# Kernel optimization log

Hardware: AMD Instinct MI355X
Metric: run time of the kernel (lower is better)

Reference implementation:

```python
import jax, jax.numpy as jnp
import numpy as np


def setup_inputs() -> dict:
    key = jax.random.key(0)
    ks = jax.random.split(key, 16)
    B, T, H = 64, 512, 256
    s = lambda n: 1.0 / np.sqrt(n)
    return {
        "q_vec": jax.random.normal(ks[0], (B, H), jnp.float32),
        "fact_vecs": jax.random.normal(ks[1], (B, T, H), jnp.float32),
        "input_len": jax.random.randint(ks[2], (B,), 1, T + 1, jnp.int32),
        "W1": jax.random.normal(ks[3], (7 * H, H), jnp.float32) * s(7 * H),
        "b1": jnp.zeros((H,), jnp.float32),
        "W2": jax.random.normal(ks[4], (H, 1), jnp.float32) * s(H),
        "b2": jnp.zeros((1,), jnp.float32),
        "Wr": jax.random.normal(ks[5], (H, H), jnp.float32) * s(H),
        "Ur": jax.random.normal(ks[6], (H, H), jnp.float32) * s(H),
        "br": jnp.zeros((H,), jnp.float32),
        "Wh": jax.random.normal(ks[7], (H, H), jnp.float32) * s(H),
        "Uh": jax.random.normal(ks[8], (H, H), jnp.float32) * s(H),
        "bh": jnp.zeros((H,), jnp.float32),
        "Ws": jax.random.normal(ks[9], (2 * H, 1), jnp.float32) * s(2 * H),
        "bs": jnp.zeros((1,), jnp.float32),
        "We": jax.random.normal(ks[10], (2 * H, 1), jnp.float32) * s(2 * H),
        "be": jnp.zeros((1,), jnp.float32),
    }


def reference(q_vec, fact_vecs, input_len, W1, b1, W2, b2,
              Wr, Ur, br, Wh, Uh, bh, Ws, bs, We, be):
    B, T, H = fact_vecs.shape
    m = q_vec  # prev_memory = q_vec (never actually updated in the original inference loop)
    qb = jnp.broadcast_to(q_vec[:, None, :], (B, T, H))
    mb = qb  # m == q_vec
    f = fact_vecs
    # episodic attention features: [f, m, q, f*q, f*m, |f-q|, |f-m|] -> [B,T,7H]
    feats = jnp.concatenate(
        [f, mb, qb, f * qb, f * mb, jnp.abs(f - qb), jnp.abs(f - mb)], axis=-1)
    att = jnp.tanh(feats @ W1 + b1) @ W2 + b2          # [B,T,1]
    g = jax.nn.softmax(att[..., 0], axis=1)            # [B,T]

    # AttentionGRU scan over time with sequence-length masking (dynamic_rnn semantics)
    valid = (jnp.arange(T)[:, None] < input_len[None, :])  # [T,B]

    def step(h, inp):
        x_t, g_t, v_t = inp  # [B,H], [B], [B]
        r = jax.nn.sigmoid(x_t @ Wr + h @ Ur + br)
        hc = jnp.tanh(x_t @ Wh + (r * h) @ Uh + bh)
        hn = g_t[:, None] * hc + (1.0 - g_t[:, None]) * h
        hn = jnp.where(v_t[:, None], hn, h)
        out = jnp.where(v_t[:, None], hn, jnp.zeros_like(hn))
        return hn, out

    xs = (jnp.swapaxes(fact_vecs, 0, 1), g.T, valid)
    _, outs = jax.lax.scan(step, jnp.zeros((B, H), fact_vecs.dtype), xs)
    e_outputs = jnp.swapaxes(outs, 0, 1)               # [B,T,H]

    # predict_position (final hop, is_iteration=False): tanh dense over [prev_memory, e_t]
    cat = jnp.concatenate([jnp.broadcast_to(m[:, None, :], (B, T, H)), e_outputs], axis=-1)
    out_s = jnp.tanh(cat @ Ws + bs)[..., 0]            # [B,T]
    out_e = jnp.tanh(cat @ We + be)[..., 0]            # [B,T]
    return out_s, out_e
```

## Files before the change

### kernel.cpp

```cpp
#include <hip/hip_runtime.h>
#include <cstddef>


static __device__ __forceinline__ float b2f(unsigned short u) {
  return __uint_as_float(((unsigned)u) << 16);
}
static __device__ __forceinline__ float blo(unsigned w) { return __uint_as_float(w << 16); }
static __device__ __forceinline__ float bhi(unsigned w) { return __uint_as_float(w & 0xffff0000u); }
static __device__ __forceinline__ unsigned short f2b(float f) {
  unsigned u = __float_as_uint(f);
  u += 0x7fffu + ((u >> 16) & 1u);
  return (unsigned short)(u >> 16);
}
static __device__ __forceinline__ float ldf(const void* b, size_t i, int md) {
  return md ? ((const float*)b)[i] : b2f(((const unsigned short*)b)[i]);
}
static __device__ __forceinline__ unsigned short ldb(const void* b, size_t i, int md) {
  return md ? f2b(((const float*)b)[i]) : ((const unsigned short*)b)[i];
}

typedef short bfrag __attribute__((ext_vector_type(8)));
typedef float f32x4 __attribute__((ext_vector_type(4)));

template <int CTRL>
static __device__ __forceinline__ float dpp_add(float x) {
  int v = __builtin_amdgcn_update_dpp(0, __float_as_int(x), CTRL, 0xF, 0xF, true);
  return x + __int_as_float(v);
}
static __device__ __forceinline__ float red16(float x) {
  x = dpp_add<0xB1>(x);
  x = dpp_add<0x4E>(x);
  x = dpp_add<0x141>(x);
  x = dpp_add<0x140>(x);
  return x;
}
static __device__ __forceinline__ void sync_lds() {
  __builtin_amdgcn_fence(__ATOMIC_RELEASE, "workgroup", "local");
  __builtin_amdgcn_s_barrier();
  __builtin_amdgcn_fence(__ATOMIC_ACQUIRE, "workgroup", "local");
}
static __device__ __forceinline__ float fast_tanh(float x) {
  float xc = fminf(fmaxf(x, -15.f), 15.f);
  return 1.f - 2.f * __builtin_amdgcn_rcpf(__expf(2.f * xc) + 1.f);
}

__global__ void k_detect(const void* __restrict__ fact, int* __restrict__ mode) {
  int tid = threadIdx.x;
  const unsigned short* u = (const unsigned short*)fact;
  float v = fabsf(b2f(u[2 * tid]));
  if (!(v == v)) v = 1e30f;
  for (int o = 32; o > 0; o >>= 1) v = fmaxf(v, __shfl_xor(v, o));
  __shared__ float red[4];
  int wave = tid >> 6, lane = tid & 63;
  if (lane == 0) red[wave] = v;
  __syncthreads();
  if (tid == 0) {
    float m = fmaxf(fmaxf(red[0], red[1]), fmaxf(red[2], red[3]));
    mode[0] = (m > 1e4f) ? 1 : 0;
  }
}

__global__ void k_prep_w(const void* __restrict__ W1,
                         const void* __restrict__ Wr,
                         const void* __restrict__ Wh,
                         const void* __restrict__ Ur,
                         const void* __restrict__ Uh,
                         const int* __restrict__ mode,
                         unsigned* __restrict__ W5q,
                         unsigned* __restrict__ Urp,
                         unsigned* __restrict__ Uhp) {
  int md = *mode;
  int idx = blockIdx.x * 256 + threadIdx.x;
  int i = idx >> 8, j = idx & 255;
  Urp[idx] = (unsigned)ldb(Ur, (size_t)(2 * i) * 256 + j, md) |
             ((unsigned)ldb(Ur, (size_t)(2 * i + 1) * 256 + j, md) << 16);
  Uhp[idx] = (unsigned)ldb(Uh, (size_t)(2 * i) * 256 + j, md) |
             ((unsigned)ldb(Uh, (size_t)(2 * i + 1) * 256 + j, md) << 16);
  float v0, v1;
  int p;
  p = i;
  v0 = ldf(W1, (size_t)(2 * i) * 256 + j, md);
  v1 = ldf(W1, (size_t)(2 * i + 1) * 256 + j, md);
  W5q[(((p >> 2) * 256 + j) << 2) + (p & 3)] = (unsigned)f2b(v0) | ((unsigned)f2b(v1) << 16);
  p = 128 + i;
  v0 = ldf(W1, (size_t)(768 + 2 * i) * 256 + j, md) + ldf(W1, (size_t)(1024 + 2 * i) * 256 + j, md);
  v1 = ldf(W1, (size_t)(769 + 2 * i) * 256 + j, md) + ldf(W1, (size_t)(1025 + 2 * i) * 256 + j, md);
  W5q[(((p >> 2) * 256 + j) << 2) + (p & 3)] = (unsigned)f2b(v0) | ((unsigned)f2b(v1) << 16);
  p = 256 + i;
  v0 = ldf(W1, (size_t)(1280 + 2 * i) * 256 + j, md) + ldf(W1, (size_t)(1536 + 2 * i) * 256 + j, md);
  v1 = ldf(W1, (size_t)(1281 + 2 * i) * 256 + j, md) + ldf(W1, (size_t)(1537 + 2 * i) * 256 + j, md);
  W5q[(((p >> 2) * 256 + j) << 2) + (p & 3)] = (unsigned)f2b(v0) | ((unsigned)f2b(v1) << 16);
  p = 384 + i;
  v0 = ldf(Wr, (size_t)(2 * i) * 256 + j, md);
  v1 = ldf(Wr, (size_t)(2 * i + 1) * 256 + j, md);
  W5q[(((p >> 2) * 256 + j) << 2) + (p & 3)] = (unsigned)f2b(v0) | ((unsigned)f2b(v1) << 16);
  p = 512 + i;
  v0 = ldf(Wh, (size_t)(2 * i) * 256 + j, md);
  v1 = ldf(Wh, (size_t)(2 * i + 1) * 256 + j, md);
  W5q[(((p >> 2) * 256 + j) << 2) + (p & 3)] = (unsigned)f2b(v0) | ((unsigned)f2b(v1) << 16);
}

__global__ void k_prep_q(const void* __restrict__ q,
                         const void* __restrict__ W1,
                         const void* __restrict__ b1,
                         const void* __restrict__ Ws,
                         const void* __restrict__ bs,
                         const void* __restrict__ We,
                         const void* __restrict__ be,
                         const int* __restrict__ mode,
                         float* __restrict__ qw1,
                         float* __restrict__ qs,
                         float* __restrict__ qe) {
  __shared__ float qsh[256];
  __shared__ float reds[4], rede[4];
  int md = *mode;
  int b = blockIdx.x, tid = threadIdx.x;
  float qv = ldf(q, (size_t)b * 256 + tid, md);
  qsh[tid] = qv;
  __syncthreads();
  float acc = ldf(b1, tid, md);
  for (int i = 0; i < 256; ++i) {
    float w = ldf(W1, (size_t)(256 + i) * 256 + tid, md) + ldf(W1, (size_t)(512 + i) * 256 + tid, md);
    acc = fmaf(qsh[i], w, acc);
  }
  qw1[b * 256 + tid] = acc;
  float ps = qv * ldf(Ws, tid, md);
  float pe = qv * ldf(We, tid, md);
  for (int o = 32; o > 0; o >>= 1) { ps += __shfl_down(ps, o); pe += __shfl_down(pe, o); }
  int wave = tid >> 6, lane = tid & 63;
  if (lane == 0) { reds[wave] = ps; rede[wave] = pe; }
  __syncthreads();
  if (tid == 0) {
    qs[b] = ldf(bs, 0, md) + reds[0] + reds[1] + reds[2] + reds[3];
    qe[b] = ldf(be, 0, md) + rede[0] + rede[1] + rede[2] + rede[3];
  }
}

__launch_bounds__(256, 2)
__global__ void k_main(const void* __restrict__ fact,
                       const void* __restrict__ q,
                       const unsigned* __restrict__ W5q,
                       const float* __restrict__ qw1,
                       const void* __restrict__ W2,
                       const void* __restrict__ b2v,
                       const void* __restrict__ br,
                       const void* __restrict__ bh,
                       const int* __restrict__ mode,
                       float* __restrict__ att,
                       unsigned* __restrict__ xrh) {
  __shared__ __align__(16) unsigned short A[16 * 776];
  __shared__ float wsc[64];
  int md = *mode;
  int blk = blockIdx.x;
  int b = blk >> 5, t0 = (blk & 31) * 16;
  int tid = threadIdx.x;
  {
    float qv = ldf(q, (size_t)b * 256 + tid, md);
    for (int r = 0; r < 16; ++r) {
      float f = ldf(fact, ((size_t)(b * 512 + t0 + r)) * 256 + tid, md);
      A[r * 776 + tid] = f2b(f);
      A[r * 776 + 256 + tid] = f2b(f * qv);
      A[r * 776 + 512 + tid] = f2b(fabsf(f - qv));
    }
  }
  __syncthreads();
  int wv = tid >> 6, lane = tid & 63;
  int n16 = lane & 15, quad = lane >> 4;
  int colb = wv * 64 + n16;
  const uint4* W4 = (const uint4*)W5q;
  f32x4 z = {0.f, 0.f, 0.f, 0.f};
  f32x4 u[4] = {z, z, z, z}, ar[4] = {z, z, z, z}, ah[4] = {z, z, z, z};
#pragma unroll
  for (int kc = 0; kc < 8; ++kc) {
    uint4 av = *(const uint4*)((const char*)A + n16 * 1552 + kc * 64 + quad * 16);
    bfrag af = __builtin_bit_cast(bfrag, av);
    int pg = kc * 4 + quad;
#pragma unroll
    for (int tile = 0; tile < 4; ++tile) {
      int col = colb + tile * 16;
      uint4 bu = W4[(size_t)pg * 256 + col];
      uint4 bw = W4[(size_t)(96 + pg) * 256 + col];
      uint4 bv = W4[(size_t)(128 + pg) * 256 + col];
      u[tile] = __builtin_amdgcn_mfma_f32_16x16x32_bf16(af, __builtin_bit_cast(bfrag, bu), u[tile], 0, 0, 0);
      ar[tile] = __builtin_amdgcn_mfma_f32_16x16x32_bf16(af, __builtin_bit_cast(bfrag, bw), ar[tile], 0, 0, 0);
      ah[tile] = __builtin_amdgcn_mfma_f32_16x16x32_bf16(af, __builtin_bit_cast(bfrag, bv), ah[tile], 0, 0, 0);
    }
  }
#pragma unroll
  for (int kc = 8; kc < 24; ++kc) {
    uint4 av = *(const uint4*)((const char*)A + n16 * 1552 + kc * 64 + quad * 16);
    bfrag af = __builtin_bit_cast(bfrag, av);
    int pg = kc * 4 + quad;
#pragma unroll
    for (int tile = 0; tile < 4; ++tile) {
      int col = colb + tile * 16;
      uint4 bu = W4[(size_t)pg * 256 + col];
      u[tile] = __builtin_amdgcn_mfma_f32_16x16x32_bf16(af, __builtin_bit_cast(bfrag, bu), u[tile], 0, 0, 0);
    }
  }
  float qwv[4], w2v[4], brv[4], bhv[4];
#pragma unroll
  for (int tile = 0; tile < 4; ++tile) {
    int col = colb + tile * 16;
    qwv[tile] = qw1[b * 256 + col];
    w2v[tile] = ldf(W2, col, md);
    brv[tile] = ldf(br, col, md);
    bhv[tile] = ldf(bh, col, md);
  }
  float ps[4];
#pragma unroll
  for (int reg = 0; reg < 4; ++reg) {
    float p = 0.f;
#pragma unroll
    for (int tile = 0; tile < 4; ++tile) {
      float hid = fast_tanh(u[tile][reg] + qwv[tile]);
      p = fmaf(hid, w2v[tile], p);
    }
    ps[reg] = red16(p);
  }
  if (n16 == 0) {
#pragma unroll
    for (int reg = 0; reg < 4; ++reg) wsc[wv * 16 + quad * 4 + reg] = ps[reg];
  }
  __syncthreads();
  if (tid < 16) {
    att[b * 512 + t0 + tid] =
        wsc[tid] + wsc[16 + tid] + wsc[32 + tid] + wsc[48 + tid] + ldf(b2v, 0, md);
  }
#pragma unroll
  for (int tile = 0; tile < 4; ++tile) {
    int col = colb + tile * 16;
#pragma unroll
    for (int reg = 0; reg < 4; ++reg) {
      int t = t0 + quad * 4 + reg;
      unsigned v = (unsigned)f2b(ar[tile][reg] + brv[tile]) |
                   ((unsigned)f2b(ah[tile][reg] + bhv[tile]) << 16);
      xrh[((size_t)(b * 512 + t)) * 256 + col] = v;
    }
  }
}

__global__ void k_softmax(const float* __restrict__ att, float* __restrict__ g) {
  __shared__ float red[8];
  int b = blockIdx.x, tid = threadIdx.x;
  float v = att[b * 512 + tid];
  float m = v;
  for (int o = 32; o > 0; o >>= 1) m = fmaxf(m, __shfl_xor(m, o));
  int wave = tid >> 6, lane = tid & 63;
  if (lane == 0) red[wave] = m;
  __syncthreads();
  m = red[0];
#pragma unroll
  for (int w = 1; w < 8; ++w) m = fmaxf(m, red[w]);
  float e = __expf(v - m);
  float s = e;
  for (int o = 32; o > 0; o >>= 1) s += __shfl_xor(s, o);
  __syncthreads();
  if (lane == 0) red[wave] = s;
  __syncthreads();
  s = red[0] + red[1] + red[2] + red[3] + red[4] + red[5] + red[6] + red[7];
  g[b * 512 + tid] = e / s;
}

__launch_bounds__(512, 2)
__global__ void k_scan(const unsigned* __restrict__ Urp,
                       const unsigned* __restrict__ Uhp,
                       const unsigned* __restrict__ xrh,
                       const float* __restrict__ g,
                       const int* __restrict__ input_len,
                       unsigned short* __restrict__ ep) {
  __shared__ __align__(16) unsigned short hB[4 * 272];
  __shared__ __align__(16) unsigned short rhB[4 * 272];
  int b0 = blockIdx.x * 4;
  int tid = threadIdx.x;
  int wv = tid >> 6, lane = tid & 63;
  int n16 = lane & 15, quad = lane >> 4;
  int col0 = wv * 32 + n16;
  int col1 = col0 + 16;
  uint4 br4[2][8], bh4[2][8];
#pragma unroll
  for (int tile = 0; tile < 2; ++tile) {
    int col = wv * 32 + tile * 16 + n16;
#pragma unroll
    for (int kc = 0; kc < 8; ++kc) {
      int p = kc * 16 + quad * 4;
      uint4 rv = {Urp[(size_t)p * 256 + col], Urp[(size_t)(p + 1) * 256 + col],
                  Urp[(size_t)(p + 2) * 256 + col], Urp[(size_t)(p + 3) * 256 + col]};
      uint4 hv = {Uhp[(size_t)p * 256 + col], Uhp[(size_t)(p + 1) * 256 + col],
                  Uhp[(size_t)(p + 2) * 256 + col], Uhp[(size_t)(p + 3) * 256 + col]};
      br4[tile][kc] = rv;
      bh4[tile][kc] = hv;
    }
  }
  for (int i = tid; i < 4 * 272; i += 512) { hB[i] = 0; rhB[i] = 0; }
  int mylen = input_len[b0 + quad];
  float hm0 = 0.f, hm1 = 0.f;
  const char* hbase = (const char*)hB + (n16 >> 2) * 544 + quad * 16;
  const char* rhbase = (const char*)rhB + (n16 >> 2) * 544 + quad * 16;
  const unsigned* xrow = xrh + (size_t)(b0 + quad) * 512 * 256;
  const float* grow = g + (size_t)(b0 + quad) * 512;
  unsigned short* eprow = ep + (size_t)(b0 + quad) * 512 * 256;

  unsigned xa[16], xbb[16];
  float4 ga0, ga1, gb0, gb1;
  auto prefetch = [&](int tb, unsigned (&xr)[16], float4& g0, float4& g1) {
    const unsigned* xp = xrow + (size_t)tb * 8 * 256;
#pragma unroll
    for (int s = 0; s < 8; ++s) {
      xr[2 * s] = xp[s * 256 + col0];
      xr[2 * s + 1] = xp[s * 256 + col1];
    }
    const float* gp = grow + tb * 8;
    g0 = *(const float4*)gp;
    g1 = *(const float4*)(gp + 4);
  };
  prefetch(0, xa, ga0, ga1);
  __syncthreads();
  const f32x4 z4 = {0.f, 0.f, 0.f, 0.f};

  auto step = [&](int T, unsigned XC0, unsigned XC1, float GT) {
    f32x4 accA[2][4];
#pragma unroll
    for (int tl = 0; tl < 2; ++tl)
#pragma unroll
      for (int j = 0; j < 4; ++j) accA[tl][j] = z4;
#pragma unroll
    for (int kc = 0; kc < 8; ++kc) {
      uint4 av = *(const uint4*)(hbase + kc * 64);
      bfrag af = __builtin_bit_cast(bfrag, av);
      int j = kc & 3;
      accA[0][j] = __builtin_amdgcn_mfma_f32_16x16x32_bf16(af, __builtin_bit_cast(bfrag, br4[0][kc]), accA[0][j], 0, 0, 0);
      accA[1][j] = __builtin_amdgcn_mfma_f32_16x16x32_bf16(af, __builtin_bit_cast(bfrag, br4[1][kc]), accA[1][j], 0, 0, 0);
    }
    {
      float v0 = (accA[0][0][0] + accA[0][1][0]) + (accA[0][2][0] + accA[0][3][0]);
      float v1 = (accA[1][0][0] + accA[1][1][0]) + (accA[1][2][0] + accA[1][3][0]);
      float e0 = __expf(-(v0 + blo(XC0)));
      float e1 = __expf(-(v1 + blo(XC1)));
      float r0 = __builtin_amdgcn_rcpf(1.f + e0);
      float r1 = __builtin_amdgcn_rcpf(1.f + e1);
      rhB[quad * 272 + col0] = f2b(r0 * hm0);
      rhB[quad * 272 + col1] = f2b(r1 * hm1);
    }
    sync_lds();
    f32x4 accB[2][4];
#pragma unroll
    for (int tl = 0; tl < 2; ++tl)
#pragma unroll
      for (int j = 0; j < 4; ++j) accB[tl][j] = z4;
#pragma unroll
    for (int kc = 0; kc < 8; ++kc) {
      uint4 av = *(const uint4*)(rhbase + kc * 64);
      bfrag af = __builtin_bit_cast(bfrag, av);
      int j = kc & 3;
      accB[0][j] = __builtin_amdgcn_mfma_f32_16x16x32_bf16(af, __builtin_bit_cast(bfrag, bh4[0][kc]), accB[0][j], 0, 0, 0);
      accB[1][j] = __builtin_amdgcn_mfma_f32_16x16x32_bf16(af, __builtin_bit_cast(bfrag, bh4[1][kc]), accB[1][j], 0, 0, 0);
    }
    {
      float w0 = (accB[0][0][0] + accB[0][1][0]) + (accB[0][2][0] + accB[0][3][0]);
      float w1 = (accB[1][0][0] + accB[1][1][0]) + (accB[1][2][0] + accB[1][3][0]);
      float c0 = fminf(fmaxf(w0 + bhi(XC0), -15.f), 15.f);
      float c1 = fminf(fmaxf(w1 + bhi(XC1), -15.f), 15.f);
      float hc0 = 1.f - 2.f * __builtin_amdgcn_rcpf(__expf(2.f * c0) + 1.f);
      float hc1 = 1.f - 2.f * __builtin_amdgcn_rcpf(__expf(2.f * c1) + 1.f);
      bool valid = T < mylen;
      float hn0 = hm0 + GT * (hc0 - hm0);
      float hn1 = hm1 + GT * (hc1 - hm1);
      hm0 = valid ? hn0 : hm0;
      hm1 = valid ? hn1 : hm1;
      unsigned short hb0 = f2b(hm0), hb1 = f2b(hm1);
      hB[quad * 272 + col0] = hb0;
      hB[quad * 272 + col1] = hb1;
      eprow[(size_t)T * 256 + col0] = valid ? hb0 : (unsigned short)0;
      eprow[(size_t)T * 256 + col1] = valid ? hb1 : (unsigned short)0;
    }
    sync_lds();
  };

  for (int tb2 = 0; tb2 < 32; ++tb2) {
    prefetch(2 * tb2 + 1, xbb, gb0, gb1);
#pragma unroll
    for (int tt = 0; tt < 8; ++tt)
      step(tb2 * 16 + tt, xa[2 * tt], xa[2 * tt + 1], tt < 4 ? ga0[tt] : ga1[tt - 4]);
    prefetch(tb2 < 31 ? 2 * tb2 + 2 : 63, xa, ga0, ga1);
#pragma unroll
    for (int tt = 0; tt < 8; ++tt)
      step(tb2 * 16 + 8 + tt, xbb[2 * tt], xbb[2 * tt + 1], tt < 4 ? gb0[tt] : gb1[tt - 4]);
  }
}

__global__ void k_out(const unsigned short* __restrict__ ep,
                      const void* __restrict__ Ws,
                      const void* __restrict__ We,
                      const float* __restrict__ qs,
                      const float* __restrict__ qe,
                      const int* __restrict__ mode,
                      float* __restrict__ out) {
  int md = *mode;
  int tid = threadIdx.x;
  int wave = tid >> 6, lane = tid & 63;
  int row = blockIdx.x * 4 + wave;
  const unsigned short* er = ep + (size_t)row * 256 + lane * 4;
  float f0 = b2f(er[0]), f1 = b2f(er[1]), f2 = b2f(er[2]), f3 = b2f(er[3]);
  int n = 256 + lane * 4;
  float s = f0 * ldf(Ws, n, md) + f1 * ldf(Ws, n + 1, md) + f2 * ldf(Ws, n + 2, md) + f3 * ldf(Ws, n + 3, md);
  float e = f0 * ldf(We, n, md) + f1 * ldf(We, n + 1, md) + f2 * ldf(We, n + 2, md) + f3 * ldf(We, n + 3, md);
  for (int o = 32; o > 0; o >>= 1) { s += __shfl_down(s, o); e += __shfl_down(e, o); }
  if (lane == 0) {
    int b = row >> 9;
    out[row] = tanhf(qs[b] + s);
    out[32768 + row] = tanhf(qe[b] + e);
  }
}

extern "C" void kernel_launch(void* const* d_in, const int* in_sizes, int n_in,
                              void* d_out, int out_size, void* d_ws, size_t ws_size,
                              hipStream_t stream) {
  const void* q    = d_in[0];
  const void* fact = d_in[1];
  const int* ilen  = (const int*)d_in[2];
  const void* W1   = d_in[3];
  const void* b1   = d_in[4];
  const void* W2   = d_in[5];
  const void* b2v  = d_in[6];
  const void* Wr   = d_in[7];
  const void* Ur   = d_in[8];
  const void* br   = d_in[9];
  const void* Wh   = d_in[10];
  const void* Uh   = d_in[11];
  const void* bh   = d_in[12];
  const void* Ws   = d_in[13];
  const void* bs   = d_in[14];
  const void* We   = d_in[15];
  const void* be   = d_in[16];

  char* w = (char*)d_ws;
  unsigned* W5q = (unsigned*)(w);
  unsigned* Urp = (unsigned*)(w + 1310720);
  unsigned* Uhp = (unsigned*)(w + 1441792);
  float*    qw1 = (float*)(w + 1572864);
  float*    qs  = (float*)(w + 1638400);
  float*    qe  = (float*)(w + 1638656);
  float*    att = (float*)(w + 1638912);
  float*    g   = (float*)(w + 1769984);
  unsigned* xrh = (unsigned*)(w + 1901056);
  unsigned short* ep = (unsigned short*)(w + 35455488);
  int*      mode = (int*)(w + 52232704);
  float* out = (float*)d_out;

  k_detect<<<dim3(1), dim3(256), 0, stream>>>(fact, mode);
  k_prep_w<<<dim3(128), dim3(256), 0, stream>>>(W1, Wr, Wh, Ur, Uh, mode, W5q, Urp, Uhp);
  k_prep_q<<<dim3(64), dim3(256), 0, stream>>>(q, W1, b1, Ws, bs, We, be, mode, qw1, qs, qe);
  k_main<<<dim3(2048), dim3(256), 0, stream>>>(fact, q, W5q, qw1, W2, b2v, br, bh, mode, att, xrh);
  k_softmax<<<dim3(64), dim3(512), 0, stream>>>(att, g);
  k_scan<<<dim3(16), dim3(512), 0, stream>>>(Urp, Uhp, xrh, g, ilen, ep);
  k_out<<<dim3(8192), dim3(256), 0, stream>>>(ep, Ws, We, qs, qe, mode, out);
}
```

Before: 678.0 us.

## Halve scan block to 4 waves, each covering 64 hidden columns

The recurrent scan kernel now runs 256 threads per block, so each wave handles four 16-column tiles instead of two. The Ur/Uh weight fragments held in registers double, and the accumulation uses two partial accumulators per tile instead of four. Fewer waves should make the two per-step LDS barriers cheaper and reuse each loaded h fragment across more MFMAs. The cost is more serial MFMA work per wave on the critical path and higher register pressure, which could cause spills.

```diff
diff --git a/kernel.cpp b/kernel.cpp
--- a/kernel.cpp
+++ b/kernel.cpp
@@ -262,7 +262,7 @@
   g[b * 512 + tid] = e / s;
 }
 
-__launch_bounds__(512, 2)
+__launch_bounds__(256, 1)
 __global__ void k_scan(const unsigned* __restrict__ Urp,
                        const unsigned* __restrict__ Uhp,
                        const unsigned* __restrict__ xrh,
@@ -275,12 +275,11 @@
   int tid = threadIdx.x;
   int wv = tid >> 6, lane = tid & 63;
   int n16 = lane & 15, quad = lane >> 4;
-  int col0 = wv * 32 + n16;
-  int col1 = col0 + 16;
-  uint4 br4[2][8], bh4[2][8];
-#pragma unroll
-  for (int tile = 0; tile < 2; ++tile) {
-    int col = wv * 32 + tile * 16 + n16;
+  int colb = wv * 64 + n16;
+  uint4 br4[4][8], bh4[4][8];
+#pragma unroll
+  for (int tile = 0; tile < 4; ++tile) {
+    int col = colb + tile * 16;
 #pragma unroll
     for (int kc = 0; kc < 8; ++kc) {
       int p = kc * 16 + quad * 4;
@@ -292,9 +291,9 @@
       bh4[tile][kc] = hv;
     }
   }
-  for (int i = tid; i < 4 * 272; i += 512) { hB[i] = 0; rhB[i] = 0; }
+  for (int i = tid; i < 4 * 272; i += 256) { hB[i] = 0; rhB[i] = 0; }
   int mylen = input_len[b0 + quad];
-  float hm0 = 0.f, hm1 = 0.f;
+  float hm[4] = {0.f, 0.f, 0.f, 0.f};
   const char* hbase = (const char*)hB + (n16 >> 2) * 544 + quad * 16;
   const char* rhbase = (const char*)rhB + (n16 >> 2) * 544 + quad * 16;
   const unsigned* xrow = xrh + (size_t)(b0 + quad) * 512 * 256;
@@ -302,90 +301,78 @@
   unsigned short* eprow = ep + (size_t)(b0 + quad) * 512 * 256;
 
   unsigned xa[16], xbb[16];
-  float4 ga0, ga1, gb0, gb1;
-  auto prefetch = [&](int tb, unsigned (&xr)[16], float4& g0, float4& g1) {
-    const unsigned* xp = xrow + (size_t)tb * 8 * 256;
-#pragma unroll
-    for (int s = 0; s < 8; ++s) {
-      xr[2 * s] = xp[s * 256 + col0];
-      xr[2 * s + 1] = xp[s * 256 + col1];
-    }
-    const float* gp = grow + tb * 8;
-    g0 = *(const float4*)gp;
-    g1 = *(const float4*)(gp + 4);
+  float4 ga, gb;
+  auto prefetch = [&](int tb, unsigned (&xr)[16], float4& gq) {
+    const unsigned* xp = xrow + (size_t)tb * 4 * 256;
+#pragma unroll
+    for (int s = 0; s < 4; ++s)
+#pragma unroll
+      for (int tl = 0; tl < 4; ++tl)
+        xr[s * 4 + tl] = xp[s * 256 + colb + tl * 16];
+    gq = *(const float4*)(grow + tb * 4);
   };
-  prefetch(0, xa, ga0, ga1);
+  prefetch(0, xa, ga);
   __syncthreads();
   const f32x4 z4 = {0.f, 0.f, 0.f, 0.f};
 
-  auto step = [&](int T, unsigned XC0, unsigned XC1, float GT) {
-    f32x4 accA[2][4];
-#pragma unroll
-    for (int tl = 0; tl < 2; ++tl)
-#pragma unroll
-      for (int j = 0; j < 4; ++j) accA[tl][j] = z4;
+  auto step = [&](int T, unsigned X0, unsigned X1, unsigned X2, unsigned X3, float GT) {
+    unsigned XC[4] = {X0, X1, X2, X3};
+    f32x4 accA[4][2];
+#pragma unroll
+    for (int tl = 0; tl < 4; ++tl) { accA[tl][0] = z4; accA[tl][1] = z4; }
 #pragma unroll
     for (int kc = 0; kc < 8; ++kc) {
       uint4 av = *(const uint4*)(hbase + kc * 64);
       bfrag af = __builtin_bit_cast(bfrag, av);
-      int j = kc & 3;
-      accA[0][j] = __builtin_amdgcn_mfma_f32_16x16x32_bf16(af, __builtin_bit_cast(bfrag, br4[0][kc]), accA[0][j], 0, 0, 0);
-      accA[1][j] = __builtin_amdgcn_mfma_f32_16x16x32_bf16(af, __builtin_bit_cast(bfrag, br4[1][kc]), accA[1][j], 0, 0, 0);
-    }
-    {
-      float v0 = (accA[0][0][0] + accA[0][1][0]) + (accA[0][2][0] + accA[0][3][0]);
-      float v1 = (accA[1][0][0] + accA[1][1][0]) + (accA[1][2][0] + accA[1][3][0]);
-      float e0 = __expf(-(v0 + blo(XC0)));
-      float e1 = __expf(-(v1 + blo(XC1)));
-      float r0 = __builtin_amdgcn_rcpf(1.f + e0);
-      float r1 = __builtin_amdgcn_rcpf(1.f + e1);
-      rhB[quad * 272 + col0] = f2b(r0 * hm0);
-      rhB[quad * 272 + col1] = f2b(r1 * hm1);
+      int j = kc & 1;
+#pragma unroll
+      for (int tl = 0; tl < 4; ++tl)
+        accA[tl][j] = __builtin_amdgcn_mfma_f32_16x16x32_bf16(af, __builtin_bit_cast(bfrag, br4[tl][kc]), accA[tl][j], 0, 0, 0);
+    }
+#pragma unroll
+    for (int tl = 0; tl < 4; ++tl) {
+      float v = accA[tl][0][0] + accA[tl][1][0];
+      float e = __expf(-(v + blo(XC[tl])));
+      float r = __builtin_amdgcn_rcpf(1.f + e);
+      rhB[quad * 272 + colb + tl * 16] = f2b(r * hm[tl]);
     }
     sync_lds();
-    f32x4 accB[2][4];
-#pragma unroll
-    for (int tl = 0; tl < 2; ++tl)
-#pragma unroll
-      for (int j = 0; j < 4; ++j) accB[tl][j] = z4;
+    f32x4 accB[4][2];
+#pragma unroll
+    for (int tl = 0; tl < 4; ++tl) { accB[tl][0] = z4; accB[tl][1] = z4; }
 #pragma unroll
     for (int kc = 0; kc < 8; ++kc) {
       uint4 av = *(const uint4*)(rhbase + kc * 64);
       bfrag af = __builtin_bit_cast(bfrag, av);
-      int j = kc & 3;
-      accB[0][j] = __builtin_amdgcn_mfma_f32_16x16x32_bf16(af, __builtin_bit_cast(bfrag, bh4[0][kc]), accB[0][j], 0, 0, 0);
-      accB[1][j] = __builtin_amdgcn_mfma_f32_16x16x32_bf16(af, __builtin_bit_cast(bfrag, bh4[1][kc]), accB[1][j], 0, 0, 0);
-    }
-    {
-      float w0 = (accB[0][0][0] + accB[0][1][0]) + (accB[0][2][0] + accB[0][3][0]);
-      float w1 = (accB[1][0][0] + accB[1][1][0]) + (accB[1][2][0] + accB[1][3][0]);
-      float c0 = fminf(fmaxf(w0 + bhi(XC0), -15.f), 15.f);
-      float c1 = fminf(fmaxf(w1 + bhi(XC1), -15.f), 15.f);
-      float hc0 = 1.f - 2.f * __builtin_amdgcn_rcpf(__expf(2.f * c0) + 1.f);
-      float hc1 = 1.f - 2.f * __builtin_amdgcn_rcpf(__expf(2.f * c1) + 1.f);
-      bool valid = T < mylen;
-      float hn0 = hm0 + GT * (hc0 - hm0);
-      float hn1 = hm1 + GT * (hc1 - hm1);
-      hm0 = valid ? hn0 : hm0;
-      hm1 = valid ? hn1 : hm1;
-      unsigned short hb0 = f2b(hm0), hb1 = f2b(hm1);
-      hB[quad * 272 + col0] = hb0;
-      hB[quad * 272 + col1] = hb1;
-      eprow[(size_t)T * 256 + col0] = valid ? hb0 : (unsigned short)0;
-      eprow[(size_t)T * 256 + col1] = valid ? hb1 : (unsigned short)0;
+      int j = kc & 1;
+#pragma unroll
+      for (int tl = 0; tl < 4; ++tl)
+        accB[tl][j] = __builtin_amdgcn_mfma_f32_16x16x32_bf16(af, __builtin_bit_cast(bfrag, bh4[tl][kc]), accB[tl][j], 0, 0, 0);
+    }
+    bool valid = T < mylen;
+#pragma unroll
+    for (int tl = 0; tl < 4; ++tl) {
+      float w = accB[tl][0][0] + accB[tl][1][0];
+      float c = fminf(fmaxf(w + bhi(XC[tl]), -15.f), 15.f);
+      float hc = 1.f - 2.f * __builtin_amdgcn_rcpf(__expf(2.f * c) + 1.f);
+      float hn = hm[tl] + GT * (hc - hm[tl]);
+      hm[tl] = valid ? hn : hm[tl];
+      unsigned short hb = f2b(hm[tl]);
+      hB[quad * 272 + colb + tl * 16] = hb;
+      eprow[(size_t)T * 256 + colb + tl * 16] = valid ? hb : (unsigned short)0;
     }
     sync_lds();
   };
 
-  for (int tb2 = 0; tb2 < 32; ++tb2) {
-    prefetch(2 * tb2 + 1, xbb, gb0, gb1);
-#pragma unroll
-    for (int tt = 0; tt < 8; ++tt)
-      step(tb2 * 16 + tt, xa[2 * tt], xa[2 * tt + 1], tt < 4 ? ga0[tt] : ga1[tt - 4]);
-    prefetch(tb2 < 31 ? 2 * tb2 + 2 : 63, xa, ga0, ga1);
-#pragma unroll
-    for (int tt = 0; tt < 8; ++tt)
-      step(tb2 * 16 + 8 + tt, xbb[2 * tt], xbb[2 * tt + 1], tt < 4 ? gb0[tt] : gb1[tt - 4]);
+  for (int tb2 = 0; tb2 < 64; ++tb2) {
+    prefetch(2 * tb2 + 1, xbb, gb);
+#pragma unroll
+    for (int s = 0; s < 4; ++s)
+      step(tb2 * 8 + s, xa[s * 4], xa[s * 4 + 1], xa[s * 4 + 2], xa[s * 4 + 3], ga[s]);
+    prefetch(tb2 < 63 ? 2 * tb2 + 2 : 127, xa, ga);
+#pragma unroll
+    for (int s = 0; s < 4; ++s)
+      step(tb2 * 8 + 4 + s, xbb[s * 4], xbb[s * 4 + 1], xbb[s * 4 + 2], xbb[s * 4 + 3], gb[s]);
   }
 }
 
@@ -453,6 +440,6 @@
   k_prep_q<<<dim3(64), dim3(256), 0, stream>>>(q, W1, b1, Ws, bs, We, be, mode, qw1, qs, qe);
   k_main<<<dim3(2048), dim3(256), 0, stream>>>(fact, q, W5q, qw1, W2, b2v, br, bh, mode, att, xrh);
   k_softmax<<<dim3(64), dim3(512), 0, stream>>>(att, g);
-  k_scan<<<dim3(16), dim3(512), 0, stream>>>(Urp, Uhp, xrh, g, ilen, ep);
+  k_scan<<<dim3(16), dim3(256), 0, stream>>>(Urp, Uhp, xrh, g, ilen, ep);
   k_out<<<dim3(8192), dim3(256), 0, stream>>>(ep, Ws, We, qs, qe, mode, out);
 }
```

Result: slower. 883.8 us (+30.4%).
